# Kernel tuning notes

Hardware: AMD Instinct MI355X
Metric: run time of the kernel (lower is better)

Reference implementation:

```python
import jax, jax.numpy as jnp
import numpy as np

N, C, T, F = 32, 64, 256, 64  # batch, EEG channels, time samples, freq bands


def setup_inputs() -> dict:
    key = jax.random.key(0)
    X = jax.random.normal(key, (N, C, T, F), dtype=jnp.float32)
    gammad = jnp.zeros((), dtype=jnp.float32)  # learned scalar, init 'zeros'
    return {"X": X, "gammad": gammad}


def reference(X, gammad):
    # X: (N, C, T, F) -> (N, F, C, T)
    Xp = jnp.transpose(X, (0, 3, 1, 2))
    # squared norms per channel: (N, F, C, 1)
    R = jnp.sum(Xp * Xp, axis=-1, keepdims=True)
    # Gram matrix over time axis: (N, F, C, C)
    G = jnp.einsum('nfct,nfkt->nfck', Xp, Xp)
    # pairwise squared Euclidean distances between channels
    D = R - 2.0 * G + jnp.swapaxes(R, -1, -2)
    # strictly-upper-triangular entries (excludes diagonal), per (n, f)
    iu, ju = jnp.triu_indices(D.shape[-1], k=1)
    triu = jnp.sqrt(D[..., iu, ju])  # (N, F, C*(C-1)/2)
    # median bandwidth (tfp.stats.percentile q=50 uses 'nearest' interpolation)
    sigma = jnp.quantile(triu, 0.5, axis=-1, method='nearest')  # (N, F)
    denom = 2.0 * jnp.power(10.0, gammad) * jnp.square(sigma)   # (N, F)
    A = jnp.exp(-D / denom[..., None, None])  # (N, F, C, C) RBF affinity
    return A
```

## Files before the change

kernel.cpp:

```cpp
#include <hip/hip_runtime.h>
#include <stdint.h>

typedef _Float16 f16x8 __attribute__((ext_vector_type(8)));
typedef float f32x4 __attribute__((ext_vector_type(4)));

__device__ __forceinline__ uint32_t pack2(float a, float b) {
    union { _Float16 h[2]; uint32_t u; } p;
    p.h[0] = (_Float16)a; p.h[1] = (_Float16)b;
    return p.u;
}

__device__ __forceinline__ f32x4 MF(f16x8 a, f16x8 b, f32x4 c) {
    return __builtin_amdgcn_mfma_f32_16x16x32_f16(a, b, c, 0, 0, 0);
}

__global__ __launch_bounds__(512, 4)
void gfc_main(const float* __restrict__ X, const float* __restrict__ gp,
              float* __restrict__ out) {
    __shared__ __align__(16) unsigned char XS[65536];
    __shared__ uint32_t histc[4][256];
    __shared__ uint32_t histf[4][128];
    __shared__ float Rbuf[4][64];

    int j = blockIdx.x;
    int xcd = j & 7, s = j >> 3;
    int gi = s >> 2, fq4 = s & 3;
    int g = gi * 8 + xcd;
    int n = g >> 2, f16g = g & 3;
    int f0 = f16g * 16 + fq4 * 4;

    int tid = threadIdx.x;
    int wid = tid >> 6, lane = tid & 63;
    int w4 = wid & 3, hi = wid >> 2;
    int l4 = lane & 15, lg = lane >> 4;

    float p10 = exp2f(gp[0] * 3.3219280948873623f);

    {
        uint32_t* hz = &histc[0][0];
        hz[tid] = 0; hz[512 + tid] = 0;
        (&histf[0][0])[tid] = 0;
    }

    const float* Xn = X + (size_t)n * 1048576 + f0;

    f32x4 dd[2][4];
    #pragma unroll
    for (int a = 0; a < 2; ++a)
        #pragma unroll
        for (int b = 0; b < 4; ++b) dd[a][b] = f32x4{0, 0, 0, 0};

    #pragma unroll
    for (int ch = 0; ch < 2; ++ch) {
        if (ch) __syncthreads();
        const float* Xc = Xn + ch * 8192;
        #pragma unroll
        for (int bt = 0; bt < 2; ++bt) {
            float4 v[4][2];
            #pragma unroll
            for (int i = 0; i < 4; ++i) {
                int c = (bt * 4 + i) * 8 + wid;
                const float* p = Xc + (size_t)c * 16384 + lane * 128;
                v[i][0] = *(const float4*)p;
                v[i][1] = *(const float4*)(p + 64);
            }
            #pragma unroll
            for (int i = 0; i < 4; ++i) {
                int c = (bt * 4 + i) * 8 + wid;
                int o = c * 256 + ((lane * 4) ^ ((c & 7) << 4));
                *(uint32_t*)(XS + o)         = pack2(v[i][0].x, v[i][1].x);
                *(uint32_t*)(XS + 16384 + o) = pack2(v[i][0].y, v[i][1].y);
                *(uint32_t*)(XS + 32768 + o) = pack2(v[i][0].z, v[i][1].z);
                *(uint32_t*)(XS + 49152 + o) = pack2(v[i][0].w, v[i][1].w);
            }
        }
        __syncthreads();

        const unsigned char* bp = XS + w4 * 16384;
        #pragma unroll
        for (int ks = 0; ks < 4; ++ks) {
            f16x8 fr[4];
            #pragma unroll
            for (int i2 = 0; i2 < 4; ++i2)
                fr[i2] = *(const f16x8*)(bp + (i2 * 16 + l4) * 256 +
                                         ((ks * 64 + lg * 16) ^ ((l4 & 7) << 4)));
            if (!hi) {
                #pragma unroll
                for (int tj = 0; tj < 4; ++tj) {
                    dd[0][tj] = MF(fr[tj], fr[0], dd[0][tj]);
                    dd[1][tj] = MF(fr[tj], fr[1], dd[1][tj]);
                }
            } else {
                #pragma unroll
                for (int tj = 0; tj < 4; ++tj) {
                    dd[0][tj] = MF(fr[tj], fr[2], dd[0][tj]);
                    dd[1][tj] = MF(fr[tj], fr[3], dd[1][tj]);
                }
            }
        }
    }

    {
        f32x4 dg0 = hi ? dd[0][2] : dd[0][0];
        f32x4 dg1 = hi ? dd[1][3] : dd[1][1];
        if (lg == (l4 >> 2)) {
            int r = l4 & 3;
            float v0 = r == 0 ? dg0[0] : r == 1 ? dg0[1] : r == 2 ? dg0[2] : dg0[3];
            float v1 = r == 0 ? dg1[0] : r == 1 ? dg1[1] : r == 2 ? dg1[2] : dg1[3];
            Rbuf[w4][(hi * 2) * 16 + l4] = v0;
            Rbuf[w4][(hi * 2 + 1) * 16 + l4] = v1;
        }
    }
    __syncthreads();

    float Rr0 = Rbuf[w4][(hi * 2) * 16 + l4];
    float Rr1 = Rbuf[w4][(hi * 2 + 1) * 16 + l4];
    #pragma unroll
    for (int tj = 0; tj < 4; ++tj) {
        f32x4 Rc = *(const f32x4*)&Rbuf[w4][tj * 16 + lg * 4];
        #pragma unroll
        for (int r = 0; r < 4; ++r) {
            dd[0][tj][r] = Rr0 + Rc[r] - 2.0f * dd[0][tj][r];
            dd[1][tj][r] = Rr1 + Rc[r] - 2.0f * dd[1][tj][r];
        }
    }

    uint32_t* hc = histc[w4];
    #pragma unroll
    for (int tt = 0; tt < 2; ++tt) {
        int row = (hi * 2 + tt) * 16 + l4;
        #pragma unroll
        for (int tj = 0; tj < 4; ++tj)
            #pragma unroll
            for (int r = 0; r < 4; ++r) {
                int col = tj * 16 + lg * 4 + r;
                if (row < col) {
                    _Float16 hx = (_Float16)fmaxf(dd[tt][tj][r], 0.0f);
                    uint32_t kb = (uint32_t)__builtin_bit_cast(uint16_t, hx);
                    atomicAdd(&hc[kb >> 7], 1u);
                }
            }
    }
    __syncthreads();

    int B, tf;
    {
        uint4 hh = *(const uint4*)&hc[lane * 4];
        int sB = (int)(hh.x + hh.y + hh.z + hh.w);
        int incl = sB;
        #pragma unroll
        for (int off = 1; off < 64; off <<= 1) {
            int t = __shfl_up(incl, off, 64);
            if (lane >= off) incl += t;
        }
        unsigned long long bal = __ballot(incl >= 1009);
        int L = __ffsll(bal) - 1;
        int inclL = __shfl(incl, L, 64);
        int a0 = __shfl((int)hh.x, L, 64);
        int a1 = __shfl((int)hh.y, L, 64);
        int a2 = __shfl((int)hh.z, L, 64);
        int a3 = __shfl((int)hh.w, L, 64);
        int excl = inclL - (a0 + a1 + a2 + a3);
        int cum;
        if (excl + a0 >= 1009)                { B = L * 4;     cum = excl; }
        else if (excl + a0 + a1 >= 1009)      { B = L * 4 + 1; cum = excl + a0; }
        else if (excl + a0 + a1 + a2 >= 1009) { B = L * 4 + 2; cum = excl + a0 + a1; }
        else                                  { B = L * 4 + 3; cum = excl + a0 + a1 + a2; }
        tf = 1009 - cum;
    }

    uint32_t* hf = histf[w4];
    #pragma unroll
    for (int tt = 0; tt < 2; ++tt) {
        int row = (hi * 2 + tt) * 16 + l4;
        #pragma unroll
        for (int tj = 0; tj < 4; ++tj)
            #pragma unroll
            for (int r = 0; r < 4; ++r) {
                int col = tj * 16 + lg * 4 + r;
                if (row < col) {
                    _Float16 hx = (_Float16)fmaxf(dd[tt][tj][r], 0.0f);
                    uint32_t kb = (uint32_t)__builtin_bit_cast(uint16_t, hx);
                    if ((int)(kb >> 7) == B) atomicAdd(&hf[kb & 127], 1u);
                }
            }
    }
    __syncthreads();

    float sigma2;
    {
        uint2 gg = *(const uint2*)&hf[lane * 2];
        int s2 = (int)(gg.x + gg.y);
        int incl = s2;
        #pragma unroll
        for (int off = 1; off < 64; off <<= 1) {
            int t = __shfl_up(incl, off, 64);
            if (lane >= off) incl += t;
        }
        unsigned long long bal = __ballot(incl >= tf);
        int L2 = __ffsll(bal) - 1;
        int inclL = __shfl(incl, L2, 64);
        int b0 = __shfl((int)gg.x, L2, 64);
        int b1 = __shfl((int)gg.y, L2, 64);
        int excl = inclL - (b0 + b1);
        int F = (excl + b0 >= tf) ? L2 * 2 : L2 * 2 + 1;
        uint16_t v15 = (uint16_t)((B << 7) | F);
        sigma2 = (float)__builtin_bit_cast(_Float16, v15);
    }
    float ninv = -1.0f / (2.0f * p10 * sigma2);

    float* op = out + ((size_t)(n * 64 + f0 + w4) << 12);
    #pragma unroll
    for (int tt = 0; tt < 2; ++tt) {
        int row = (hi * 2 + tt) * 16 + l4;
        #pragma unroll
        for (int tj = 0; tj < 4; ++tj) {
            float4 rv;
            rv.x = __expf(dd[tt][tj][0] * ninv);
            rv.y = __expf(dd[tt][tj][1] * ninv);
            rv.z = __expf(dd[tt][tj][2] * ninv);
            rv.w = __expf(dd[tt][tj][3] * ninv);
            *(float4*)(op + row * 64 + tj * 16 + lg * 4) = rv;
        }
    }
}

extern "C" void kernel_launch(void* const* d_in, const int* in_sizes, int n_in,
                              void* d_out, int out_size, void* d_ws, size_t ws_size,
                              hipStream_t stream) {
    (void)in_sizes; (void)n_in; (void)out_size; (void)d_ws; (void)ws_size;
    const float* X  = (const float*)d_in[0];
    const float* gp = (const float*)d_in[1];
    float* out = (float*)d_out;
    gfc_main<<<512, 512, 0, stream>>>(X, gp, out);
}
```

Before: 63.17 us.

## Prefetch second time chunk during first Gram pass and use bitwise radix-select median

```diff
diff --git a/kernel.cpp b/kernel.cpp
--- a/kernel.cpp
+++ b/kernel.cpp
@@ -14,12 +14,35 @@
     return __builtin_amdgcn_mfma_f32_16x16x32_f16(a, b, c, 0, 0, 0);
 }
 
+__device__ __forceinline__ void gram_chunk(const unsigned char* bp, f32x4 dd[2][4],
+                                           int l4, int lg, int hi) {
+    #pragma unroll
+    for (int ks = 0; ks < 4; ++ks) {
+        f16x8 fr[4];
+        #pragma unroll
+        for (int i2 = 0; i2 < 4; ++i2)
+            fr[i2] = *(const f16x8*)(bp + (i2 * 16 + l4) * 256 +
+                                     ((ks * 64 + lg * 16) ^ ((l4 & 7) << 4)));
+        if (!hi) {
+            #pragma unroll
+            for (int tj = 0; tj < 4; ++tj) {
+                dd[0][tj] = MF(fr[tj], fr[0], dd[0][tj]);
+                dd[1][tj] = MF(fr[tj], fr[1], dd[1][tj]);
+            }
+        } else {
+            #pragma unroll
+            for (int tj = 0; tj < 4; ++tj) {
+                dd[0][tj] = MF(fr[tj], fr[2], dd[0][tj]);
+                dd[1][tj] = MF(fr[tj], fr[3], dd[1][tj]);
+            }
+        }
+    }
+}
+
 __global__ __launch_bounds__(512, 4)
 void gfc_main(const float* __restrict__ X, const float* __restrict__ gp,
               float* __restrict__ out) {
     __shared__ __align__(16) unsigned char XS[65536];
-    __shared__ uint32_t histc[4][256];
-    __shared__ uint32_t histf[4][128];
     __shared__ float Rbuf[4][64];
 
     int j = blockIdx.x;
@@ -36,69 +59,62 @@
 
     float p10 = exp2f(gp[0] * 3.3219280948873623f);
 
+    const float* Xn = X + (size_t)n * 1048576 + f0;
+
+    f32x4 dd[2][4];
+    #pragma unroll
+    for (int a = 0; a < 2; ++a)
+        #pragma unroll
+        for (int b = 0; b < 4; ++b) dd[a][b] = f32x4{0, 0, 0, 0};
+
     {
-        uint32_t* hz = &histc[0][0];
-        hz[tid] = 0; hz[512 + tid] = 0;
-        (&histf[0][0])[tid] = 0;
-    }
-
-    const float* Xn = X + (size_t)n * 1048576 + f0;
-
-    f32x4 dd[2][4];
-    #pragma unroll
-    for (int a = 0; a < 2; ++a)
-        #pragma unroll
-        for (int b = 0; b < 4; ++b) dd[a][b] = f32x4{0, 0, 0, 0};
-
-    #pragma unroll
-    for (int ch = 0; ch < 2; ++ch) {
-        if (ch) __syncthreads();
-        const float* Xc = Xn + ch * 8192;
-        #pragma unroll
-        for (int bt = 0; bt < 2; ++bt) {
-            float4 v[4][2];
-            #pragma unroll
-            for (int i = 0; i < 4; ++i) {
-                int c = (bt * 4 + i) * 8 + wid;
-                const float* p = Xc + (size_t)c * 16384 + lane * 128;
-                v[i][0] = *(const float4*)p;
-                v[i][1] = *(const float4*)(p + 64);
-            }
-            #pragma unroll
-            for (int i = 0; i < 4; ++i) {
-                int c = (bt * 4 + i) * 8 + wid;
-                int o = c * 256 + ((lane * 4) ^ ((c & 7) << 4));
-                *(uint32_t*)(XS + o)         = pack2(v[i][0].x, v[i][1].x);
-                *(uint32_t*)(XS + 16384 + o) = pack2(v[i][0].y, v[i][1].y);
-                *(uint32_t*)(XS + 32768 + o) = pack2(v[i][0].z, v[i][1].z);
-                *(uint32_t*)(XS + 49152 + o) = pack2(v[i][0].w, v[i][1].w);
-            }
-        }
-        __syncthreads();
-
-        const unsigned char* bp = XS + w4 * 16384;
-        #pragma unroll
-        for (int ks = 0; ks < 4; ++ks) {
-            f16x8 fr[4];
-            #pragma unroll
-            for (int i2 = 0; i2 < 4; ++i2)
-                fr[i2] = *(const f16x8*)(bp + (i2 * 16 + l4) * 256 +
-                                         ((ks * 64 + lg * 16) ^ ((l4 & 7) << 4)));
-            if (!hi) {
-                #pragma unroll
-                for (int tj = 0; tj < 4; ++tj) {
-                    dd[0][tj] = MF(fr[tj], fr[0], dd[0][tj]);
-                    dd[1][tj] = MF(fr[tj], fr[1], dd[1][tj]);
-                }
-            } else {
-                #pragma unroll
-                for (int tj = 0; tj < 4; ++tj) {
-                    dd[0][tj] = MF(fr[tj], fr[2], dd[0][tj]);
-                    dd[1][tj] = MF(fr[tj], fr[3], dd[1][tj]);
-                }
-            }
-        }
-    }
+        float4 v[8][2];
+        #pragma unroll
+        for (int k = 0; k < 8; ++k) {
+            int c = k * 8 + wid;
+            const float* p = Xn + (size_t)c * 16384 + lane * 128;
+            v[k][0] = *(const float4*)p;
+            v[k][1] = *(const float4*)(p + 64);
+        }
+        #pragma unroll
+        for (int k = 0; k < 8; ++k) {
+            int c = k * 8 + wid;
+            int o = c * 256 + ((lane * 4) ^ ((c & 7) << 4));
+            *(uint32_t*)(XS + o)         = pack2(v[k][0].x, v[k][1].x);
+            *(uint32_t*)(XS + 16384 + o) = pack2(v[k][0].y, v[k][1].y);
+            *(uint32_t*)(XS + 32768 + o) = pack2(v[k][0].z, v[k][1].z);
+            *(uint32_t*)(XS + 49152 + o) = pack2(v[k][0].w, v[k][1].w);
+        }
+    }
+
+    float4 pv[8][2];
+    #pragma unroll
+    for (int k = 0; k < 8; ++k) {
+        int c = k * 8 + wid;
+        const float* p = Xn + 8192 + (size_t)c * 16384 + lane * 128;
+        pv[k][0] = *(const float4*)p;
+        pv[k][1] = *(const float4*)(p + 64);
+    }
+
+    __syncthreads();
+
+    gram_chunk(XS + w4 * 16384, dd, l4, lg, hi);
+
+    __syncthreads();
+
+    #pragma unroll
+    for (int k = 0; k < 8; ++k) {
+        int c = k * 8 + wid;
+        int o = c * 256 + ((lane * 4) ^ ((c & 7) << 4));
+        *(uint32_t*)(XS + o)         = pack2(pv[k][0].x, pv[k][1].x);
+        *(uint32_t*)(XS + 16384 + o) = pack2(pv[k][0].y, pv[k][1].y);
+        *(uint32_t*)(XS + 32768 + o) = pack2(pv[k][0].z, pv[k][1].z);
+        *(uint32_t*)(XS + 49152 + o) = pack2(pv[k][0].w, pv[k][1].w);
+    }
+
+    __syncthreads();
+
+    gram_chunk(XS + w4 * 16384, dd, l4, lg, hi);
 
     {
         f32x4 dg0 = hi ? dd[0][2] : dd[0][0];
@@ -115,6 +131,7 @@
 
     float Rr0 = Rbuf[w4][(hi * 2) * 16 + l4];
     float Rr1 = Rbuf[w4][(hi * 2 + 1) * 16 + l4];
+    int keys[64];
     #pragma unroll
     for (int tj = 0; tj < 4; ++tj) {
         f32x4 Rc = *(const f32x4*)&Rbuf[w4][tj * 16 + lg * 4];
@@ -124,8 +141,6 @@
             dd[1][tj][r] = Rr1 + Rc[r] - 2.0f * dd[1][tj][r];
         }
     }
-
-    uint32_t* hc = histc[w4];
     #pragma unroll
     for (int tt = 0; tt < 2; ++tt) {
         int row = (hi * 2 + tt) * 16 + l4;
@@ -134,79 +149,36 @@
             #pragma unroll
             for (int r = 0; r < 4; ++r) {
                 int col = tj * 16 + lg * 4 + r;
-                if (row < col) {
-                    _Float16 hx = (_Float16)fmaxf(dd[tt][tj][r], 0.0f);
-                    uint32_t kb = (uint32_t)__builtin_bit_cast(uint16_t, hx);
-                    atomicAdd(&hc[kb >> 7], 1u);
-                }
+                _Float16 hx = (_Float16)fmaxf(dd[tt][tj][r], 0.0f);
+                uint16_t kb = __builtin_bit_cast(uint16_t, hx);
+                keys[tt * 16 + tj * 4 + r] = (row < col) ? (int)kb : 0x7FFF;
             }
     }
-    __syncthreads();
-
-    int B, tf;
+
     {
-        uint4 hh = *(const uint4*)&hc[lane * 4];
-        int sB = (int)(hh.x + hh.y + hh.z + hh.w);
-        int incl = sB;
-        #pragma unroll
-        for (int off = 1; off < 64; off <<= 1) {
-            int t = __shfl_up(incl, off, 64);
-            if (lane >= off) incl += t;
-        }
-        unsigned long long bal = __ballot(incl >= 1009);
-        int L = __ffsll(bal) - 1;
-        int inclL = __shfl(incl, L, 64);
-        int a0 = __shfl((int)hh.x, L, 64);
-        int a1 = __shfl((int)hh.y, L, 64);
-        int a2 = __shfl((int)hh.z, L, 64);
-        int a3 = __shfl((int)hh.w, L, 64);
-        int excl = inclL - (a0 + a1 + a2 + a3);
-        int cum;
-        if (excl + a0 >= 1009)                { B = L * 4;     cum = excl; }
-        else if (excl + a0 + a1 >= 1009)      { B = L * 4 + 1; cum = excl + a0; }
-        else if (excl + a0 + a1 + a2 >= 1009) { B = L * 4 + 2; cum = excl + a0 + a1; }
-        else                                  { B = L * 4 + 3; cum = excl + a0 + a1 + a2; }
-        tf = 1009 - cum;
-    }
-
-    uint32_t* hf = histf[w4];
-    #pragma unroll
-    for (int tt = 0; tt < 2; ++tt) {
-        int row = (hi * 2 + tt) * 16 + l4;
-        #pragma unroll
-        for (int tj = 0; tj < 4; ++tj)
-            #pragma unroll
-            for (int r = 0; r < 4; ++r) {
-                int col = tj * 16 + lg * 4 + r;
-                if (row < col) {
-                    _Float16 hx = (_Float16)fmaxf(dd[tt][tj][r], 0.0f);
-                    uint32_t kb = (uint32_t)__builtin_bit_cast(uint16_t, hx);
-                    if ((int)(kb >> 7) == B) atomicAdd(&hf[kb & 127], 1u);
-                }
-            }
-    }
-    __syncthreads();
-
-    float sigma2;
-    {
-        uint2 gg = *(const uint2*)&hf[lane * 2];
-        int s2 = (int)(gg.x + gg.y);
-        int incl = s2;
-        #pragma unroll
-        for (int off = 1; off < 64; off <<= 1) {
-            int t = __shfl_up(incl, off, 64);
-            if (lane >= off) incl += t;
-        }
-        unsigned long long bal = __ballot(incl >= tf);
-        int L2 = __ffsll(bal) - 1;
-        int inclL = __shfl(incl, L2, 64);
-        int b0 = __shfl((int)gg.x, L2, 64);
-        int b1 = __shfl((int)gg.y, L2, 64);
-        int excl = inclL - (b0 + b1);
-        int F = (excl + b0 >= tf) ? L2 * 2 : L2 * 2 + 1;
-        uint16_t v15 = (uint16_t)((B << 7) | F);
-        sigma2 = (float)__builtin_bit_cast(_Float16, v15);
-    }
+        unsigned char* base = XS + w4 * 16384;
+        uint16_t* mywr = (uint16_t*)(base + hi * 4096);
+        #pragma unroll
+        for (int e = 0; e < 32; ++e)
+            mywr[e * 64 + lane] = (uint16_t)keys[e];
+        __syncthreads();
+        const uint16_t* prd = (const uint16_t*)(base + (hi ^ 1) * 4096);
+        #pragma unroll
+        for (int e = 0; e < 32; ++e)
+            keys[32 + e] = (int)prd[e * 64 + lane];
+    }
+
+    int u = 0;
+    for (int bit = 14; bit >= 0; --bit) {
+        int cand = u | (1 << bit);
+        int cnt = 0;
+        #pragma unroll
+        for (int i = 0; i < 64; ++i) cnt += (keys[i] < cand) ? 1 : 0;
+        #pragma unroll
+        for (int off = 32; off; off >>= 1) cnt += __shfl_xor(cnt, off, 64);
+        if (cnt <= 1008) u = cand;
+    }
+    float sigma2 = (float)__builtin_bit_cast(_Float16, (uint16_t)u);
     float ninv = -1.0f / (2.0f * p10 * sigma2);
 
     float* op = out + ((size_t)(n * 64 + f0 + w4) << 12);
```

Measured after the change: 77.56 us. 1.23x slower.
